# Performance work log

Measured on AMD Instinct MI355X. Metric: run time of the kernel, lower is better.

The kernel has to match this reference:

```python
import jax, jax.numpy as jnp
import numpy as np

M, K, N, G = 4096, 4096, 11008, 128


def setup_inputs() -> dict:
    key = jax.random.key(0)
    k1, k2, k3, k4, k5 = jax.random.split(key, 5)
    inp = jax.random.normal(k1, (M, K), dtype=jnp.float32)
    # int4 quantized weights, unpacked to one value per element, range [0, 16)
    qweight = jax.random.randint(k2, (K, N), 0, 16, dtype=jnp.int32)
    # group-wise scales / zero-points: one per (group along K, output column)
    scales = jax.random.uniform(k3, (K // G, N), dtype=jnp.float32, minval=0.001, maxval=0.02)
    qzeros = jax.random.randint(k4, (K // G, N), 0, 16, dtype=jnp.int32)
    bias = jax.random.normal(k5, (N,), dtype=jnp.float32) * 0.01
    return {"input": inp, "qweight": qweight, "scales": scales,
            "qzeros": qzeros, "bias": bias, "group_size": G}


def reference(input, qweight, scales, qzeros, bias, group_size):
    # Dequantize: w[k, n] = (q[k, n] - zp[k//G, n]) * scale[k//G, n]
    zp_full = jnp.repeat(qzeros.astype(jnp.float32), group_size, axis=0)   # [K, N]
    sc_full = jnp.repeat(scales, group_size, axis=0)                        # [K, N]
    w = (qweight.astype(jnp.float32) - zp_full) * sc_full                   # [K, N]
    # mm_bias_int4: out = input @ dequant(W) + bias
    return jnp.dot(input, w) + bias[None, :]
```

## Files before the change

### kernel.cpp

```cpp
#include <hip/hip_runtime.h>
#include <hip/hip_bf16.h>
#include <stdint.h>

#define MDIM 4096
#define KDIM 4096
#define NDIM 11008

typedef __bf16 bf16x8 __attribute__((ext_vector_type(8)));
typedef float  f32x4  __attribute__((ext_vector_type(4)));

__global__ __launch_bounds__(512) void int4_gemm_mfma(
    const float* __restrict__ A, const int* __restrict__ Q,
    const float* __restrict__ S, const int* __restrict__ Z,
    const float* __restrict__ bias, float* __restrict__ out)
{
    __shared__ __bf16 sA[2][256 * 32];
    __shared__ __bf16 sB[2][256 * 32];

    auto SW = [](int row, int c) -> int {
        return ((row >> 1) << 7) + (((((row & 1) << 2) | c) ^ ((row >> 1) & 7)) << 4);
    };

    const int nbm = MDIM / 256;
    const int nwg = (MDIM / 256) * (NDIM / 256);
    const int xcd = blockIdx.x & 7;
    const int wg  = xcd * (nwg >> 3) + (blockIdx.x >> 3);
    const int bm  = wg % nbm;
    const int bn  = wg / nbm;
    const int m0 = bm * 256, n0 = bn * 256;

    const int t    = threadIdx.x;
    const int lane = t & 63;
    const int wave = t >> 6;
    const int wm   = (wave >> 2) * 128;
    const int wn   = (wave & 3) * 64;
    const int fr   = lane & 15;
    const int fq   = lane >> 4;

    const int arow = t >> 1;
    const int acb  = (t & 1) * 2;
    const int bn2  = (t & 127) * 2;
    const int bko  = (t >> 7) * 8;
    const int bcc  = t >> 7;

    f32x4 acc[8][4];
    #pragma unroll
    for (int i = 0; i < 8; ++i)
        #pragma unroll
        for (int j = 0; j < 4; ++j)
            #pragma unroll
            for (int r = 0; r < 4; ++r)
                acc[i][j][r] = 0.0f;

    float4 ra0, ra1, ra2, ra3;
    int2   rq[8];
    float2 sc;
    int2   zp;

    auto LOAD = [&](int kt) {
        const int k0 = kt * 32;
        const float* ap = A + (size_t)(m0 + arow) * KDIM + k0 + (t & 1) * 16;
        ra0 = ((const float4*)ap)[0];
        ra1 = ((const float4*)ap)[1];
        ra2 = ((const float4*)ap)[2];
        ra3 = ((const float4*)ap)[3];
        #pragma unroll
        for (int j = 0; j < 8; ++j)
            rq[j] = *(const int2*)(Q + (size_t)(k0 + bko + j) * NDIM + n0 + bn2);
        if ((kt & 3) == 0) {
            const int g = kt >> 2;
            sc = *(const float2*)(S + (size_t)g * NDIM + n0 + bn2);
            zp = *(const int2*)  (Z + (size_t)g * NDIM + n0 + bn2);
        }
    };

    auto STORE = [&](int buf) {
        bf16x8 v0, v1;
        v0[0] = (__bf16)ra0.x; v0[1] = (__bf16)ra0.y;
        v0[2] = (__bf16)ra0.z; v0[3] = (__bf16)ra0.w;
        v0[4] = (__bf16)ra1.x; v0[5] = (__bf16)ra1.y;
        v0[6] = (__bf16)ra1.z; v0[7] = (__bf16)ra1.w;
        v1[0] = (__bf16)ra2.x; v1[1] = (__bf16)ra2.y;
        v1[2] = (__bf16)ra2.z; v1[3] = (__bf16)ra2.w;
        v1[4] = (__bf16)ra3.x; v1[5] = (__bf16)ra3.y;
        v1[6] = (__bf16)ra3.z; v1[7] = (__bf16)ra3.w;
        *(bf16x8*)((char*)sA[buf] + SW(arow, acb))     = v0;
        *(bf16x8*)((char*)sA[buf] + SW(arow, acb + 1)) = v1;

        const float zs0 = -(float)zp.x * sc.x;
        const float zs1 = -(float)zp.y * sc.y;
        bf16x8 w0, w1;
        #pragma unroll
        for (int j = 0; j < 8; ++j) {
            w0[j] = (__bf16)((float)rq[j].x * sc.x + zs0);
            w1[j] = (__bf16)((float)rq[j].y * sc.y + zs1);
        }
        *(bf16x8*)((char*)sB[buf] + SW(bn2,     bcc)) = w0;
        *(bf16x8*)((char*)sB[buf] + SW(bn2 + 1, bcc)) = w1;
    };

    LOAD(0);
    STORE(0);
    __syncthreads();

    for (int kt = 0; kt < KDIM / 32; ++kt) {
        const int c = kt & 1;

        if (kt < KDIM / 32 - 1) LOAD(kt + 1);

        bf16x8 aF[8], bF[4];
        #pragma unroll
        for (int i = 0; i < 8; ++i)
            aF[i] = *(const bf16x8*)((char*)sA[c] + SW(wm + 16 * i + fr, fq));
        #pragma unroll
        for (int j = 0; j < 4; ++j)
            bF[j] = *(const bf16x8*)((char*)sB[c] + SW(wn + 16 * j + fr, fq));

        #pragma unroll
        for (int i = 0; i < 8; ++i)
            #pragma unroll
            for (int j = 0; j < 4; ++j)
                acc[i][j] = __builtin_amdgcn_mfma_f32_16x16x32_bf16(
                                aF[i], bF[j], acc[i][j], 0, 0, 0);

        if (kt < KDIM / 32 - 1) STORE(c ^ 1);

        __syncthreads();
    }

    float bj[4];
    #pragma unroll
    for (int j = 0; j < 4; ++j)
        bj[j] = bias[n0 + wn + 16 * j + fr];

    #pragma unroll
    for (int i = 0; i < 8; ++i) {
        #pragma unroll
        for (int r = 0; r < 4; ++r) {
            const int m = m0 + wm + 16 * i + fq * 4 + r;
            float* op = out + (size_t)m * NDIM + n0 + wn + fr;
            #pragma unroll
            for (int j = 0; j < 4; ++j)
                op[16 * j] = acc[i][j][r] + bj[j];
        }
    }
}

extern "C" void kernel_launch(void* const* d_in, const int* in_sizes, int n_in,
                              void* d_out, int out_size, void* d_ws, size_t ws_size,
                              hipStream_t stream) {
    const float* A    = (const float*)d_in[0];
    const int*   Q    = (const int*)d_in[1];
    const float* S    = (const float*)d_in[2];
    const int*   Z    = (const int*)d_in[3];
    const float* bias = (const float*)d_in[4];
    float* out = (float*)d_out;

    const int grid = (MDIM / 256) * (NDIM / 256);
    int4_gemm_mfma<<<dim3(grid), dim3(512), 0, stream>>>(A, Q, S, Z, bias, out);
}
```

Before: 1.050 ms.

## Restructure main loop into an unrolled two-stage pipeline with early LDS stores

The K loop is unrolled by two with fixed shared-memory buffer indices. Each half reads its LDS fragments first, then converts and stores the next tile, then issues the global loads for the tile after that, so the global loads stay in flight across the MFMA block and the barrier. The MFMA block is wrapped in s_setprio to raise wave priority. The barrier waits only on LDS operations (lgkmcnt), not on outstanding global loads. Global addresses now come from pointers that are incremented each tile instead of being recomputed. In exchange, register pressure and scheduling become more fragile, and the loop relies on the compiler inserting the correct vmcnt waits before the held loads are used.

Result: faster. 895.3 us (-14.7%).

```diff
diff --git a/kernel.cpp b/kernel.cpp
--- a/kernel.cpp
+++ b/kernel.cpp
@@ -5,6 +5,7 @@
 #define MDIM 4096
 #define KDIM 4096
 #define NDIM 11008
+#define NT   (KDIM / 32)
 
 typedef __bf16 bf16x8 __attribute__((ext_vector_type(8)));
 typedef float  f32x4  __attribute__((ext_vector_type(4)));
@@ -52,26 +53,32 @@
             for (int r = 0; r < 4; ++r)
                 acc[i][j][r] = 0.0f;
 
+    const float* aP = A + (size_t)(m0 + arow) * KDIM + (t & 1) * 16;
+    const int*   qP = Q + (size_t)bko * NDIM + n0 + bn2;
+
     float4 ra0, ra1, ra2, ra3;
     int2   rq[8];
     float2 sc;
     int2   zp;
 
     auto LOAD = [&](int kt) {
-        const int k0 = kt * 32;
-        const float* ap = A + (size_t)(m0 + arow) * KDIM + k0 + (t & 1) * 16;
-        ra0 = ((const float4*)ap)[0];
-        ra1 = ((const float4*)ap)[1];
-        ra2 = ((const float4*)ap)[2];
-        ra3 = ((const float4*)ap)[3];
+        ra0 = ((const float4*)aP)[0];
+        ra1 = ((const float4*)aP)[1];
+        ra2 = ((const float4*)aP)[2];
+        ra3 = ((const float4*)aP)[3];
+        const int* q = qP;
         #pragma unroll
-        for (int j = 0; j < 8; ++j)
-            rq[j] = *(const int2*)(Q + (size_t)(k0 + bko + j) * NDIM + n0 + bn2);
+        for (int j = 0; j < 8; ++j) {
+            rq[j] = *(const int2*)q;
+            q += NDIM;
+        }
         if ((kt & 3) == 0) {
             const int g = kt >> 2;
             sc = *(const float2*)(S + (size_t)g * NDIM + n0 + bn2);
             zp = *(const int2*)  (Z + (size_t)g * NDIM + n0 + bn2);
         }
+        aP += 32;
+        qP += (size_t)32 * NDIM;
     };
 
     auto STORE = [&](int buf) {
@@ -99,33 +106,53 @@
         *(bf16x8*)((char*)sB[buf] + SW(bn2 + 1, bcc)) = w1;
     };
 
-    LOAD(0);
-    STORE(0);
-    __syncthreads();
-
-    for (int kt = 0; kt < KDIM / 32; ++kt) {
-        const int c = kt & 1;
-
-        if (kt < KDIM / 32 - 1) LOAD(kt + 1);
-
-        bf16x8 aF[8], bF[4];
+    auto FRAGS = [&](int buf, bf16x8 (&aF)[8], bf16x8 (&bF)[4]) {
         #pragma unroll
         for (int i = 0; i < 8; ++i)
-            aF[i] = *(const bf16x8*)((char*)sA[c] + SW(wm + 16 * i + fr, fq));
+            aF[i] = *(const bf16x8*)((char*)sA[buf] + SW(wm + 16 * i + fr, fq));
         #pragma unroll
         for (int j = 0; j < 4; ++j)
-            bF[j] = *(const bf16x8*)((char*)sB[c] + SW(wn + 16 * j + fr, fq));
+            bF[j] = *(const bf16x8*)((char*)sB[buf] + SW(wn + 16 * j + fr, fq));
+    };
 
+    auto MFMAS = [&](bf16x8 (&aF)[8], bf16x8 (&bF)[4]) {
+        __builtin_amdgcn_s_setprio(1);
         #pragma unroll
         for (int i = 0; i < 8; ++i)
             #pragma unroll
             for (int j = 0; j < 4; ++j)
                 acc[i][j] = __builtin_amdgcn_mfma_f32_16x16x32_bf16(
                                 aF[i], bF[j], acc[i][j], 0, 0, 0);
+        __builtin_amdgcn_s_setprio(0);
+    };
 
-        if (kt < KDIM / 32 - 1) STORE(c ^ 1);
+    auto BAR = [&]() {
+        asm volatile("s_waitcnt lgkmcnt(0)" ::: "memory");
+        __builtin_amdgcn_s_barrier();
+    };
 
-        __syncthreads();
+    LOAD(0);
+    STORE(0);
+    LOAD(1);
+    BAR();
+
+    for (int kt = 0; kt < NT; kt += 2) {
+        {
+            bf16x8 aF[8], bF[4];
+            FRAGS(0, aF, bF);
+            STORE(1);
+            if (kt + 2 < NT) LOAD(kt + 2);
+            MFMAS(aF, bF);
+            BAR();
+        }
+        {
+            bf16x8 aF[8], bF[4];
+            FRAGS(1, aF, bF);
+            if (kt + 2 < NT) STORE(0);
+            if (kt + 3 < NT) LOAD(kt + 3);
+            MFMAS(aF, bF);
+            BAR();
+        }
     }
 
     float bj[4];
```

## Stream fp32 A tiles into LDS via async loads with triple buffering

Applied to the files above, without the earlier changes.

Activation tiles are now copied directly from global memory into a three-stage fp32 LDS ring using global_load_lds, and are converted to bf16 when fragments are read, instead of being staged through registers. The weight load runs two tiles ahead, and explicit vmcnt waits with raw barriers replace __syncthreads. The wave tiling changes from 128x64 to 64x128 so each wave reads fewer A fragments, and MFMA issue is wrapped in setprio. This aims to hide global latency and cut register traffic, at the cost of double the LDS footprint for A and conversion work repeated by every wave that reads the same A row.

Measured after the change: 879.0 us. -16.3%, faster.

```diff
diff --git a/kernel.cpp b/kernel.cpp
--- a/kernel.cpp
+++ b/kernel.cpp
@@ -5,17 +5,21 @@
 #define MDIM 4096
 #define KDIM 4096
 #define NDIM 11008
+#define NT   (KDIM / 32)
 
 typedef __bf16 bf16x8 __attribute__((ext_vector_type(8)));
 typedef float  f32x4  __attribute__((ext_vector_type(4)));
+
+typedef __attribute__((address_space(1))) const void gv_t;
+typedef __attribute__((address_space(3))) void       lv_t;
 
 __global__ __launch_bounds__(512) void int4_gemm_mfma(
     const float* __restrict__ A, const int* __restrict__ Q,
     const float* __restrict__ S, const int* __restrict__ Z,
     const float* __restrict__ bias, float* __restrict__ out)
 {
-    __shared__ __bf16 sA[2][256 * 32];
-    __shared__ __bf16 sB[2][256 * 32];
+    __shared__ float  sAf[3][256 * 32];
+    __shared__ __bf16 sB [2][256 * 32];
 
     auto SW = [](int row, int c) -> int {
         return ((row >> 1) << 7) + (((((row & 1) << 2) | c) ^ ((row >> 1) & 7)) << 4);
@@ -32,61 +36,57 @@
     const int t    = threadIdx.x;
     const int lane = t & 63;
     const int wave = t >> 6;
-    const int wm   = (wave >> 2) * 128;
-    const int wn   = (wave & 3) * 64;
+    const int wm   = (wave & 3) * 64;
+    const int wn2  = (wave >> 2) * 128;
     const int fr   = lane & 15;
     const int fq   = lane >> 4;
+    const int f7   = fr & 7;
 
-    const int arow = t >> 1;
-    const int acb  = (t & 1) * 2;
     const int bn2  = (t & 127) * 2;
     const int bko  = (t >> 7) * 8;
     const int bcc  = t >> 7;
 
-    f32x4 acc[8][4];
+    f32x4 acc[4][8];
     #pragma unroll
-    for (int i = 0; i < 8; ++i)
+    for (int i = 0; i < 4; ++i)
         #pragma unroll
-        for (int j = 0; j < 4; ++j)
+        for (int j = 0; j < 8; ++j)
             #pragma unroll
             for (int r = 0; r < 4; ++r)
                 acc[i][j][r] = 0.0f;
 
-    float4 ra0, ra1, ra2, ra3;
+    const float* aGP = A + (size_t)(m0 + 32 * wave + (lane >> 3)) * KDIM
+                         + (((lane & 7) ^ (lane >> 3)) << 2);
+    const int* qP = Q + (size_t)bko * NDIM + n0 + bn2;
+
     int2   rq[8];
     float2 sc;
     int2   zp;
 
-    auto LOAD = [&](int kt) {
-        const int k0 = kt * 32;
-        const float* ap = A + (size_t)(m0 + arow) * KDIM + k0 + (t & 1) * 16;
-        ra0 = ((const float4*)ap)[0];
-        ra1 = ((const float4*)ap)[1];
-        ra2 = ((const float4*)ap)[2];
-        ra3 = ((const float4*)ap)[3];
+    auto ISSUE_A = [&](int wbuf) {
+        lv_t* dst = (lv_t*)&sAf[wbuf][wave * 1024];
         #pragma unroll
-        for (int j = 0; j < 8; ++j)
-            rq[j] = *(const int2*)(Q + (size_t)(k0 + bko + j) * NDIM + n0 + bn2);
-        if ((kt & 3) == 0) {
-            const int g = kt >> 2;
-            sc = *(const float2*)(S + (size_t)g * NDIM + n0 + bn2);
-            zp = *(const int2*)  (Z + (size_t)g * NDIM + n0 + bn2);
-        }
+        for (int i = 0; i < 4; ++i)
+            __builtin_amdgcn_global_load_lds(
+                (gv_t*)(aGP + (size_t)i * 8 * KDIM),
+                (lv_t*)((char*)dst + i * 1024), 16, 0, 0);
+        aGP += 32;
     };
 
-    auto STORE = [&](int buf) {
-        bf16x8 v0, v1;
-        v0[0] = (__bf16)ra0.x; v0[1] = (__bf16)ra0.y;
-        v0[2] = (__bf16)ra0.z; v0[3] = (__bf16)ra0.w;
-        v0[4] = (__bf16)ra1.x; v0[5] = (__bf16)ra1.y;
-        v0[6] = (__bf16)ra1.z; v0[7] = (__bf16)ra1.w;
-        v1[0] = (__bf16)ra2.x; v1[1] = (__bf16)ra2.y;
-        v1[2] = (__bf16)ra2.z; v1[3] = (__bf16)ra2.w;
-        v1[4] = (__bf16)ra3.x; v1[5] = (__bf16)ra3.y;
-        v1[6] = (__bf16)ra3.z; v1[7] = (__bf16)ra3.w;
-        *(bf16x8*)((char*)sA[buf] + SW(arow, acb))     = v0;
-        *(bf16x8*)((char*)sA[buf] + SW(arow, acb + 1)) = v1;
+    auto LOAD_Q = [&](int tile) {
+        const int* q = qP;
+        #pragma unroll
+        for (int j = 0; j < 8; ++j) {
+            rq[j] = *(const int2*)q;
+            q += NDIM;
+        }
+        const int g = tile >> 2;
+        sc = *(const float2*)(S + (size_t)g * NDIM + n0 + bn2);
+        zp = *(const int2*)  (Z + (size_t)g * NDIM + n0 + bn2);
+        qP += (size_t)32 * NDIM;
+    };
 
+    auto STORE_B = [&](int buf) {
         const float zs0 = -(float)zp.x * sc.x;
         const float zs1 = -(float)zp.y * sc.y;
         bf16x8 w0, w1;
@@ -99,48 +99,75 @@
         *(bf16x8*)((char*)sB[buf] + SW(bn2 + 1, bcc)) = w1;
     };
 
-    LOAD(0);
-    STORE(0);
-    __syncthreads();
+    LOAD_Q(0);
+    ISSUE_A(0);
+    ISSUE_A(1);
+    STORE_B(0);
+    LOAD_Q(1);
+    asm volatile("s_waitcnt vmcnt(14) lgkmcnt(0)" ::: "memory");
+    __builtin_amdgcn_s_barrier();
 
-    for (int kt = 0; kt < KDIM / 32; ++kt) {
-        const int c = kt & 1;
+    int ab = 0;
+    for (int kt = 0; kt < NT; ++kt) {
+        const char* abuf = (const char*)sAf[ab];
+        const char* bbuf = (const char*)sB[kt & 1];
 
-        if (kt < KDIM / 32 - 1) LOAD(kt + 1);
+        bf16x8 aF[4], bF[8];
+        #pragma unroll
+        for (int i = 0; i < 4; ++i) {
+            const char* rp = abuf + (size_t)(wm + 16 * i + fr) * 128;
+            f32x4 u0 = *(const f32x4*)(rp + ((( 2 * fq    ) ^ f7) << 4));
+            f32x4 u1 = *(const f32x4*)(rp + (((2 * fq + 1) ^ f7) << 4));
+            bf16x8 v;
+            v[0] = (__bf16)u0[0]; v[1] = (__bf16)u0[1];
+            v[2] = (__bf16)u0[2]; v[3] = (__bf16)u0[3];
+            v[4] = (__bf16)u1[0]; v[5] = (__bf16)u1[1];
+            v[6] = (__bf16)u1[2]; v[7] = (__bf16)u1[3];
+            aF[i] = v;
+        }
+        #pragma unroll
+        for (int j = 0; j < 8; ++j)
+            bF[j] = *(const bf16x8*)(bbuf + SW(wn2 + 16 * j + fr, fq));
 
-        bf16x8 aF[8], bF[4];
+        if (kt < NT - 1) STORE_B((kt + 1) & 1);
+        if (kt < NT - 2) {
+            LOAD_Q(kt + 2);
+            int wb = ab + 2; if (wb >= 3) wb -= 3;
+            ISSUE_A(wb);
+        }
+
+        __builtin_amdgcn_s_setprio(1);
         #pragma unroll
-        for (int i = 0; i < 8; ++i)
-            aF[i] = *(const bf16x8*)((char*)sA[c] + SW(wm + 16 * i + fr, fq));
-        #pragma unroll
-        for (int j = 0; j < 4; ++j)
-            bF[j] = *(const bf16x8*)((char*)sB[c] + SW(wn + 16 * j + fr, fq));
-
-        #pragma unroll
-        for (int i = 0; i < 8; ++i)
+        for (int i = 0; i < 4; ++i)
             #pragma unroll
-            for (int j = 0; j < 4; ++j)
+            for (int j = 0; j < 8; ++j)
                 acc[i][j] = __builtin_amdgcn_mfma_f32_16x16x32_bf16(
                                 aF[i], bF[j], acc[i][j], 0, 0, 0);
+        __builtin_amdgcn_s_setprio(0);
 
-        if (kt < KDIM / 32 - 1) STORE(c ^ 1);
-
-        __syncthreads();
+        if (kt < NT - 2) {
+            asm volatile("s_waitcnt vmcnt(14) lgkmcnt(0)" ::: "memory");
+            __builtin_amdgcn_s_barrier();
+        } else if (kt == NT - 2) {
+            asm volatile("s_waitcnt vmcnt(0) lgkmcnt(0)" ::: "memory");
+            __builtin_amdgcn_s_barrier();
+        }
+        ab = (ab == 2) ? 0 : ab + 1;
     }
 
-    float bj[4];
+    float bj[8];
     #pragma unroll
-    for (int j = 0; j < 4; ++j)
-        bj[j] = bias[n0 + wn + 16 * j + fr];
+    for (int j = 0; j < 8; ++j)
+        bj[j] = bias[n0 + wn2 + 16 * j + fr];
 
     #pragma unroll
-    for (int i = 0; i < 8; ++i) {
+    for (int i = 0; i < 4; ++i) {
         #pragma unroll
         for (int r = 0; r < 4; ++r) {
             const int m = m0 + wm + 16 * i + fq * 4 + r;
-            float* op = out + (size_t)m * NDIM + n0 + wn + fr;
+            float* op = out + (size_t)m * NDIM + n0 + wn2 + fr;
             #pragma unroll
-            for (int j = 0; j < 4; ++j)
+            for (int j = 0; j < 8; ++j)
                 op[16 * j] = acc[i][j][r] + bj[j];
         }
     }
```
